# Optimization experiments

Hardware: AMD Instinct MI355X
Metric: run time of the kernel (lower is better)

The kernel has to match this reference:

```python
import jax, jax.numpy as jnp
import numpy as np

M, A, E, H = 2048, 64, 128, 256
NUM_BOND_TYPES, NUM_ATOM_TYPES = 4, 118

def setup_inputs() -> dict:
    key = jax.random.key(0)
    ks = jax.random.split(key, 12)
    s = 0.02
    return {
        'node_rep': jax.random.normal(ks[0], (M, A, H), jnp.float32),
        'edge_index': jax.random.randint(ks[1], (M, 2, E), 0, A, jnp.int32),
        'bond_type_target': jax.random.randint(ks[2], (M, E), 0, NUM_BOND_TYPES, jnp.int32),
        'atom_type_target': jax.random.randint(ks[3], (M, A), 0, NUM_ATOM_TYPES, jnp.int32),
        'Wp1': jax.random.normal(ks[4], (H, H), jnp.float32) * s, 'bp1': jnp.zeros((H,), jnp.float32),
        'Wp2': jax.random.normal(ks[5], (H, H), jnp.float32) * s, 'bp2': jnp.zeros((H,), jnp.float32),
        'Wb1': jax.random.normal(ks[6], (2 * H, H), jnp.float32) * s, 'bb1': jnp.zeros((H,), jnp.float32),
        'Wb2': jax.random.normal(ks[7], (H, NUM_BOND_TYPES), jnp.float32) * s, 'bb2': jnp.zeros((NUM_BOND_TYPES,), jnp.float32),
        'Wa1': jax.random.normal(ks[8], (H, H), jnp.float32) * s, 'ba1': jnp.zeros((H,), jnp.float32),
        'Wa2': jax.random.normal(ks[9], (H, NUM_ATOM_TYPES), jnp.float32) * s, 'ba2': jnp.zeros((NUM_ATOM_TYPES,), jnp.float32),
    }

def _mlp(x, W1, b1, W2, b2):
    return jnp.maximum(x @ W1 + b1, 0.0) @ W2 + b2

def reference(node_rep, edge_index, bond_type_target, atom_type_target,
              Wp1, bp1, Wp2, bp2, Wb1, bb1, Wb2, bb2, Wa1, ba1, Wa2, ba2):
    # bond_if_proj: per-atom 2-layer MLP (dropout=0 -> identity)  [M,A,H]
    proj = _mlp(node_rep, Wp1, bp1, Wp2, bp2)
    # gather bond endpoint reps: index_select over atoms per molecule  [M,E,H]
    start = jnp.take_along_axis(proj, edge_index[:, 0, :, None], axis=1)
    end = jnp.take_along_axis(proj, edge_index[:, 1, :, None], axis=1)
    bt_in = jnp.concatenate([start, end], axis=-1)            # [M,E,2H]
    bt_logits = _mlp(bt_in, Wb1, bb1, Wb2, bb2)               # [M,E,4]
    bt_logp = jax.nn.log_softmax(bt_logits, axis=-1)
    # per-molecule mean CE averaged over molecules == global mean (equal sizes)
    bond_type_loss = -jnp.mean(jnp.take_along_axis(bt_logp, bond_type_target[..., None], axis=-1))
    bond_type_acc = jnp.mean((jnp.argmax(bt_logits, axis=-1) == bond_type_target).astype(jnp.float32))
    # atom type classifier on raw node reps  [M,A,118]
    at_logits = _mlp(node_rep, Wa1, ba1, Wa2, ba2)
    at_logp = jax.nn.log_softmax(at_logits, axis=-1)
    atom_type_loss = -jnp.mean(jnp.take_along_axis(at_logp, atom_type_target[..., None], axis=-1))
    atom_type_acc = jnp.mean((jnp.argmax(at_logits, axis=-1) == atom_type_target).astype(jnp.float32))
    loss = 0.5 * bond_type_loss + 0.5 * atom_type_loss
    return loss, bond_type_acc, atom_type_acc
```

## Files before the change

### kernel.cpp

```cpp
#include <hip/hip_runtime.h>
#include <hip/hip_bf16.h>

typedef __bf16 bf16x8 __attribute__((ext_vector_type(8)));
typedef float f32x16 __attribute__((ext_vector_type(16)));

__device__ inline unsigned short f2bf(float f) {
  __hip_bfloat16 h = __float2bfloat16(f);
  return *reinterpret_cast<unsigned short*>(&h);
}
__device__ inline unsigned pack2bf(float a, float b) {
  return (unsigned)f2bf(a) | ((unsigned)f2bf(b) << 16);
}
__device__ inline uint2 pack4bf(float a, float b, float c, float d) {
  uint2 r; r.x = pack2bf(a, b); r.y = pack2bf(c, d); return r;
}
__device__ inline bf16x8 as_bf16x8(uint4 v) { return __builtin_bit_cast(bf16x8, v); }
__device__ inline float bitf(unsigned u) { return __builtin_bit_cast(float, u); }
__device__ inline f32x16 mfma16(bf16x8 a, bf16x8 b, f32x16 c) {
  return __builtin_amdgcn_mfma_f32_32x32x16_bf16(a, b, c, 0, 0, 0);
}

#define BROW(XB, KK)                                                           \
  ((XB) + ((((rw + l31) << 9) + ((KK) << 5) + (h << 4)) ^ swz))

#define GEMM8(XB, W1PTR, W2PTR)                                                \
  {                                                                            \
    const unsigned char* w1_ = (const unsigned char*)(W1PTR) +                 \
                               ((cw + l31) << 5) + (h << 4);                   \
    const unsigned char* w2_ = (const unsigned char*)(W2PTR) +                 \
                               ((cw + l31) << 5) + (h << 4);                   \
    u0 = zero; u1 = zero; v0 = zero; v1 = zero;                                \
    bf16x8 pB = *(const bf16x8*)BROW(XB, 0);                                   \
    uint4 pA0 = *(const uint4*)(w1_);                                          \
    uint4 pA1 = *(const uint4*)(w1_ + 1024);                                   \
    uint4 pC0 = *(const uint4*)(w2_);                                          \
    uint4 pC1 = *(const uint4*)(w2_ + 1024);                                   \
    _Pragma("clang loop unroll(disable)")                                      \
    for (int kk = 0; kk < 16; kk += 2) {                                       \
      bf16x8 qB = *(const bf16x8*)BROW(XB, kk + 1);                            \
      uint4 qA0 = *(const uint4*)(w1_ + ((kk + 1) << 13));                     \
      uint4 qA1 = *(const uint4*)(w1_ + ((kk + 1) << 13) + 1024);              \
      uint4 qC0 = *(const uint4*)(w2_ + ((kk + 1) << 13));                     \
      uint4 qC1 = *(const uint4*)(w2_ + ((kk + 1) << 13) + 1024);              \
      u0 = mfma16(as_bf16x8(pA0), pB, u0);                                     \
      u1 = mfma16(as_bf16x8(pA1), pB, u1);                                     \
      v0 = mfma16(as_bf16x8(pC0), pB, v0);                                     \
      v1 = mfma16(as_bf16x8(pC1), pB, v1);                                     \
      if (kk + 2 < 16) {                                                       \
        pB = *(const bf16x8*)BROW(XB, kk + 2);                                 \
        pA0 = *(const uint4*)(w1_ + ((kk + 2) << 13));                         \
        pA1 = *(const uint4*)(w1_ + ((kk + 2) << 13) + 1024);                  \
        pC0 = *(const uint4*)(w2_ + ((kk + 2) << 13));                         \
        pC1 = *(const uint4*)(w2_ + ((kk + 2) << 13) + 1024);                  \
      }                                                                        \
      u0 = mfma16(as_bf16x8(qA0), qB, u0);                                     \
      u1 = mfma16(as_bf16x8(qA1), qB, u1);                                     \
      v0 = mfma16(as_bf16x8(qC0), qB, v0);                                     \
      v1 = mfma16(as_bf16x8(qC1), qB, v1);                                     \
    }                                                                          \
  }

#define WB8(DB, ACC, C, BIASPTR)                                               \
  _Pragma("unroll")                                                            \
  for (int g = 0; g < 4; ++g) {                                                \
    int xr_ = rw + l31;                                                        \
    int col = cw + (C) * 32 + g * 8 + h * 4;                                   \
    float4 bb = *(const float4*)((BIASPTR) + col);                             \
    float v0_ = fmaxf(ACC[4 * g + 0] + bb.x, 0.f);                             \
    float v1_ = fmaxf(ACC[4 * g + 1] + bb.y, 0.f);                             \
    float v2_ = fmaxf(ACC[4 * g + 2] + bb.z, 0.f);                             \
    float v3_ = fmaxf(ACC[4 * g + 3] + bb.w, 0.f);                             \
    int off = ((xr_ << 9) + (col << 1)) ^ ((xr_ & 7) << 4);                    \
    *(uint2*)((DB) + off) = pack4bf(v0_, v1_, v2_, v3_);                       \
  }

#define WB8R(DB, ACC, C)                                                       \
  _Pragma("unroll")                                                            \
  for (int g = 0; g < 4; ++g) {                                                \
    int xr_ = rw + l31;                                                        \
    int col = cw + (C) * 32 + g * 8 + h * 4;                                   \
    int off = ((xr_ << 9) + (col << 1)) ^ ((xr_ & 7) << 4);                    \
    *(uint2*)((DB) + off) = pack4bf(ACC[4 * g + 0], ACC[4 * g + 1],            \
                                    ACC[4 * g + 2], ACC[4 * g + 3]);           \
  }

#define STAGE_X(DST, SRC)                                                      \
  _Pragma("unroll")                                                            \
  for (int it = 0; it < 4; ++it) {                                             \
    int lb = (it * 512 + tid) * 16;                                            \
    int d_ = lb ^ (((lb >> 9) & 7) << 4);                                      \
    const float4* s4 = (const float4*)((SRC) + (lb >> 1));                     \
    float4 f0 = s4[0], f1 = s4[1];                                             \
    uint4 v_ = { pack2bf(f0.x, f0.y), pack2bf(f0.z, f0.w),                     \
                 pack2bf(f1.x, f1.y), pack2bf(f1.z, f1.w) };                   \
    *(uint4*)((DST) + d_) = v_;                                                \
  }

__global__ __launch_bounds__(256) void k_pack(
    const float* __restrict__ wp1, const float* __restrict__ wa1,
    const float* __restrict__ wa2,
    unsigned short* __restrict__ dp1, unsigned short* __restrict__ da1,
    unsigned short* __restrict__ da2, float* __restrict__ accum)
{
  int b = blockIdx.x, tid = threadIdx.x;
  if (b == 0 && tid < 8) accum[tid] = 0.f;
  const float* src; unsigned short* dst; int e, logN, Nreal;
  if (b < 256)       { src = wp1; dst = dp1; e = b * 256 + tid;          logN = 8; Nreal = 256; }
  else if (b < 512)  { src = wa1; dst = da1; e = (b - 256) * 256 + tid;  logN = 8; Nreal = 256; }
  else               { src = wa2; dst = da2; e = (b - 512) * 256 + tid;  logN = 7; Nreal = 118; }
  int dk = e & 15;
  int rest = e >> 4;
  int n = rest & ((1 << logN) - 1);
  int kk = rest >> logN;
  int k = kk * 16 + dk;
  float v = (n < Nreal) ? src[k * Nreal + n] : 0.f;
  dst[e] = f2bf(v);
}

__global__ __launch_bounds__(256) void k_fold(
    const float* __restrict__ wp2, const float* __restrict__ wb1,
    const float* __restrict__ bp2, const float* __restrict__ bb1,
    unsigned short* __restrict__ dct, unsigned short* __restrict__ dcb,
    float* __restrict__ bias_e)
{
  int b = blockIdx.x, n = threadIdx.x;
  if (b < 512) {
    int k = b & 255;
    int off = (b < 256) ? 0 : 256;
    float s = 0.f;
    for (int t = 0; t < 256; ++t)
      s += wp2[k * 256 + t] * wb1[(t + off) * 256 + n];
    unsigned short* dst = (b < 256) ? dct : dcb;
    dst[((k >> 4) * 256 + n) * 16 + (k & 15)] = f2bf(s);
  } else {
    float s = bb1[n];
    for (int t = 0; t < 256; ++t)
      s += bp2[t] * (wb1[t * 256 + n] + wb1[(256 + t) * 256 + n]);
    bias_e[n] = s;
  }
}

__global__ __launch_bounds__(512, 4) void k_mol(
    const float* __restrict__ node, const int* __restrict__ eidx,
    const int* __restrict__ btt, const int* __restrict__ att,
    const unsigned short* __restrict__ wp1p, const float* __restrict__ bp1,
    const unsigned short* __restrict__ wctp, const unsigned short* __restrict__ wcbp,
    const float* __restrict__ bias_e, const float* __restrict__ wb2,
    const float* __restrict__ bb2,
    const unsigned short* __restrict__ wa1p, const float* __restrict__ ba1,
    const unsigned short* __restrict__ wa2p, const float* __restrict__ ba2,
    float* __restrict__ accum)
{
  __shared__ __align__(16) unsigned char bufA[32768];
  __shared__ __align__(16) unsigned char bufB[32768];
  __shared__ float s_bias[256];
  __shared__ float4 s_wb2[256];
  __shared__ float s_b2a[128];
  __shared__ float s_red[16];
  const int tid = threadIdx.x;
  const int lane = tid & 63;
  const int w = tid >> 6;
  const int l31 = lane & 31;
  const int h = lane >> 5;
  const int swz = (l31 & 7) << 4;
  const int rw = (w >> 2) * 32;
  const int cw = (w & 3) * 64;
  const int m = blockIdx.x;

  STAGE_X(bufA, node + (long)m * 16384);
  if (tid < 256) {
    s_bias[tid] = bias_e[tid];
    s_wb2[tid] = ((const float4*)wb2)[tid];
  }
  if (tid < 128) s_b2a[tid] = (tid < 118) ? ba2[tid] : 0.f;
  const int t_at = att[m * 64 + (tid >> 3)];
  __syncthreads();

  f32x16 zero = {};
  f32x16 u0, u1, v0, v1;

  GEMM8(bufA, wa1p, wp1p);
  WB8(bufB, u0, 0, ba1);
  WB8(bufB, u1, 1, ba1);
  __syncthreads();
  WB8(bufA, v0, 0, bp1);
  WB8(bufA, v1, 1, bp1);
  __syncthreads();

  f32x16 aL = zero;
  {
    const int cw2 = (w & 3) * 32;
    const unsigned char* wb_ = (const unsigned char*)wa2p +
                               ((cw2 + l31) << 5) + (h << 4);
    bf16x8 pB = *(const bf16x8*)BROW(bufB, 0);
    uint4 pA = *(const uint4*)(wb_);
    _Pragma("clang loop unroll(disable)")
    for (int kk = 0; kk < 16; kk += 2) {
      bf16x8 qB = *(const bf16x8*)BROW(bufB, kk + 1);
      uint4 qA = *(const uint4*)(wb_ + ((kk + 1) << 12));
      aL = mfma16(as_bf16x8(pA), pB, aL);
      if (kk + 2 < 16) {
        pB = *(const bf16x8*)BROW(bufB, kk + 2);
        pA = *(const uint4*)(wb_ + ((kk + 2) << 12));
      }
      aL = mfma16(as_bf16x8(qA), qB, aL);
    }
  }
  __syncthreads();

  {
    const int cw2 = (w & 3) * 32;
    const int r0 = rw + l31;
    #pragma unroll
    for (int q = 0; q < 16; ++q) {
      int col = cw2 + (q & 3) + 8 * (q >> 2) + 4 * h;
      if (col < 118)
        *(float*)(bufB + ((r0 << 9) + (((col << 2)) ^ ((r0 & 7) << 4)))) =
            aL[q] + s_b2a[col];
    }
  }
  __syncthreads();

  {
    const int row = tid >> 3, g8 = tid & 7;
    const unsigned char* lr = bufB + (row << 9);
    const int rswz = (row & 7) << 4;
    const int c0 = g8 * 15;
    const int cend = (g8 == 7) ? 118 : c0 + 15;
    float mx = -3.0e38f; int am = 127;
    for (int c = c0; c < cend; ++c) {
      float v = *(const float*)(lr + (((c << 2)) ^ rswz));
      if (v > mx) { mx = v; am = c; }
    }
    #pragma unroll
    for (int d = 1; d < 8; d <<= 1) {
      float mo = __shfl_xor(mx, d); int amo = __shfl_xor(am, d);
      if (mo > mx || (mo == mx && amo < am)) { mx = mo; am = amo; }
    }
    float s = 0.f, vt = 0.f;
    for (int c = c0; c < cend; ++c) {
      float v = *(const float*)(lr + (((c << 2)) ^ rswz));
      s += __expf(v - mx);
      if (c == t_at) vt = v;
    }
    #pragma unroll
    for (int d = 1; d < 8; d <<= 1) { s += __shfl_xor(s, d); vt += __shfl_xor(vt, d); }
    float ce = 0.f, cc = 0.f;
    if (g8 == 0) { ce = __logf(s) + mx - vt; cc = (am == t_at) ? 1.f : 0.f; }
    #pragma unroll
    for (int d = 8; d < 64; d <<= 1) { ce += __shfl_xor(ce, d); cc += __shfl_xor(cc, d); }
    #pragma unroll
    for (int d = 1; d < 8; d <<= 1) { ce += __shfl_xor(ce, d); cc += __shfl_xor(cc, d); }
    if (lane == 0) { s_red[w * 2] = ce; s_red[w * 2 + 1] = cc; }
  }

  GEMM8(bufA, wctp, wcbp);
  const int es = eidx[m * 256 + (tid >> 2)];
  const int ed = eidx[m * 256 + 128 + (tid >> 2)];
  const int etg = btt[m * 128 + (tid >> 2)];
  const float b20 = bb2[0], b21 = bb2[1], b22 = bb2[2], b23 = bb2[3];
  __syncthreads();
  if (tid == 0) {
    atomicAdd(accum + 2, s_red[0] + s_red[2] + s_red[4] + s_red[6] +
                         s_red[8] + s_red[10] + s_red[12] + s_red[14]);
    atomicAdd(accum + 3, s_red[1] + s_red[3] + s_red[5] + s_red[7] +
                         s_red[9] + s_red[11] + s_red[13] + s_red[15]);
  }
  WB8R(bufA, u0, 0);
  WB8R(bufA, u1, 1);
  WB8R(bufB, v0, 0);
  WB8R(bufB, v1, 1);
  __syncthreads();

  {
    const int qf = tid & 3;
    float lg0 = 0.f, lg1 = 0.f, lg2 = 0.f, lg3 = 0.f;
    #pragma unroll
    for (int j = 0; j < 8; ++j) {
      int c0 = qf * 64 + j * 8;
      int offS = ((es << 9) + (c0 << 1)) ^ ((es & 7) << 4);
      int offD = ((ed << 9) + (c0 << 1)) ^ ((ed & 7) << 4);
      uint4 us = *(const uint4*)(bufA + offS);
      uint4 ud = *(const uint4*)(bufB + offD);
      const unsigned* pu = (const unsigned*)&us;
      const unsigned* pv = (const unsigned*)&ud;
      #pragma unroll
      for (int q = 0; q < 4; ++q) {
        unsigned ua = pu[q], ub = pv[q];
        int c = c0 + 2 * q;
        float hlo = bitf(ua << 16) + bitf(ub << 16) + s_bias[c];
        float hhi = bitf(ua & 0xffff0000u) + bitf(ub & 0xffff0000u) + s_bias[c + 1];
        hlo = fmaxf(hlo, 0.f); hhi = fmaxf(hhi, 0.f);
        float4 w0 = s_wb2[c], w1 = s_wb2[c + 1];
        lg0 = fmaf(hlo, w0.x, fmaf(hhi, w1.x, lg0));
        lg1 = fmaf(hlo, w0.y, fmaf(hhi, w1.y, lg1));
        lg2 = fmaf(hlo, w0.z, fmaf(hhi, w1.z, lg2));
        lg3 = fmaf(hlo, w0.w, fmaf(hhi, w1.w, lg3));
      }
    }
    lg0 += __shfl_xor(lg0, 1); lg1 += __shfl_xor(lg1, 1);
    lg2 += __shfl_xor(lg2, 1); lg3 += __shfl_xor(lg3, 1);
    lg0 += __shfl_xor(lg0, 2); lg1 += __shfl_xor(lg1, 2);
    lg2 += __shfl_xor(lg2, 2); lg3 += __shfl_xor(lg3, 2);
    float ce = 0.f, cc = 0.f;
    if (qf == 0) {
      float l0 = lg0 + b20, l1 = lg1 + b21, l2 = lg2 + b22, l3 = lg3 + b23;
      int t = etg;
      int am = 0; float mx = l0;
      if (l1 > mx) { mx = l1; am = 1; }
      if (l2 > mx) { mx = l2; am = 2; }
      if (l3 > mx) { mx = l3; am = 3; }
      float s = __expf(l0 - mx) + __expf(l1 - mx) + __expf(l2 - mx) + __expf(l3 - mx);
      float lt = (t == 0) ? l0 : (t == 1) ? l1 : (t == 2) ? l2 : l3;
      ce = __logf(s) + mx - lt;
      cc = (am == t) ? 1.f : 0.f;
    }
    #pragma unroll
    for (int d = 1; d < 64; d <<= 1) { ce += __shfl_xor(ce, d); cc += __shfl_xor(cc, d); }
    if (lane == 0) { s_red[w * 2] = ce; s_red[w * 2 + 1] = cc; }
    __syncthreads();
    if (tid == 0) {
      atomicAdd(accum + 0, s_red[0] + s_red[2] + s_red[4] + s_red[6] +
                           s_red[8] + s_red[10] + s_red[12] + s_red[14]);
      atomicAdd(accum + 1, s_red[1] + s_red[3] + s_red[5] + s_red[7] +
                           s_red[9] + s_red[11] + s_red[13] + s_red[15]);
    }
  }
}

__global__ __launch_bounds__(64) void k_final(const float* __restrict__ accum,
                                              float* __restrict__ out)
{
  if (threadIdx.x == 0) {
    float bce = accum[0] / 262144.f;
    float bcc = accum[1] / 262144.f;
    float ace = accum[2] / 131072.f;
    float acc_ = accum[3] / 131072.f;
    out[0] = 0.5f * bce + 0.5f * ace;
    out[1] = bcc;
    out[2] = acc_;
  }
}

extern "C" void kernel_launch(void* const* d_in, const int* in_sizes, int n_in,
                              void* d_out, int out_size, void* d_ws, size_t ws_size,
                              hipStream_t stream)
{
  const float* node = (const float*)d_in[0];
  const int* eidx   = (const int*)d_in[1];
  const int* btt    = (const int*)d_in[2];
  const int* att    = (const int*)d_in[3];
  const float* Wp1 = (const float*)d_in[4];
  const float* bp1 = (const float*)d_in[5];
  const float* Wp2 = (const float*)d_in[6];
  const float* bp2 = (const float*)d_in[7];
  const float* Wb1 = (const float*)d_in[8];
  const float* bb1 = (const float*)d_in[9];
  const float* Wb2 = (const float*)d_in[10];
  const float* bb2 = (const float*)d_in[11];
  const float* Wa1 = (const float*)d_in[12];
  const float* ba1 = (const float*)d_in[13];
  const float* Wa2 = (const float*)d_in[14];
  const float* ba2 = (const float*)d_in[15];

  char* ws = (char*)d_ws;
  float* accum = (float*)ws;
  unsigned short* dp1 = (unsigned short*)(ws + 256);
  unsigned short* da1 = (unsigned short*)(ws + 131328);
  unsigned short* da2 = (unsigned short*)(ws + 262400);
  unsigned short* dct = (unsigned short*)(ws + 327936);
  unsigned short* dcb = (unsigned short*)(ws + 459008);
  float* bias_e       = (float*)(ws + 590080);

  k_pack<<<640, 256, 0, stream>>>(Wp1, Wa1, Wa2, dp1, da1, da2, accum);
  k_fold<<<513, 256, 0, stream>>>(Wp2, Wb1, bp2, bb1, dct, dcb, bias_e);
  k_mol<<<2048, 512, 0, stream>>>(node, eidx, btt, att, dp1, bp1, dct, dcb,
                                  bias_e, Wb2, bb2, da1, ba1, da2, ba2, accum);
  k_final<<<1, 64, 0, stream>>>(accum, (float*)d_out);
}
```

Before: 188.6 us.

## Process two molecules per block with 1024 threads and vectorize softmax LDS access

Each block now handles two molecules (128 atom rows) with 1024 threads, doubling the LDS buffers, so each weight tile loaded from global memory is reused across twice as many rows. The atom-logit writeback and the log-softmax scans switch from scalar to float4 LDS accesses. The block now uses about 136KB of LDS and 1024 threads, which may cut residency to one block per CU and limit latency hiding. The GEMM macros use 8 waves of row/column mapping (rw from w>>2), so whether the larger tile maps correctly to 16 waves is not visible here.

```diff
diff --git a/kernel.cpp b/kernel.cpp
--- a/kernel.cpp
+++ b/kernel.cpp
@@ -87,7 +87,7 @@
 #define STAGE_X(DST, SRC)                                                      \
   _Pragma("unroll")                                                            \
   for (int it = 0; it < 4; ++it) {                                             \
-    int lb = (it * 512 + tid) * 16;                                            \
+    int lb = (it * 1024 + tid) * 16;                                           \
     int d_ = lb ^ (((lb >> 9) & 7) << 4);                                      \
     const float4* s4 = (const float4*)((SRC) + (lb >> 1));                     \
     float4 f0 = s4[0], f1 = s4[1];                                             \
@@ -140,7 +140,7 @@
   }
 }
 
-__global__ __launch_bounds__(512, 4) void k_mol(
+__global__ __launch_bounds__(1024, 4) void k_mol(
     const float* __restrict__ node, const int* __restrict__ eidx,
     const int* __restrict__ btt, const int* __restrict__ att,
     const unsigned short* __restrict__ wp1p, const float* __restrict__ bp1,
@@ -151,12 +151,12 @@
     const unsigned short* __restrict__ wa2p, const float* __restrict__ ba2,
     float* __restrict__ accum)
 {
-  __shared__ __align__(16) unsigned char bufA[32768];
-  __shared__ __align__(16) unsigned char bufB[32768];
+  __shared__ __align__(16) unsigned char bufA[65536];
+  __shared__ __align__(16) unsigned char bufB[65536];
   __shared__ float s_bias[256];
   __shared__ float4 s_wb2[256];
   __shared__ float s_b2a[128];
-  __shared__ float s_red[16];
+  __shared__ float s_red[32];
   const int tid = threadIdx.x;
   const int lane = tid & 63;
   const int w = tid >> 6;
@@ -167,13 +167,13 @@
   const int cw = (w & 3) * 64;
   const int m = blockIdx.x;
 
-  STAGE_X(bufA, node + (long)m * 16384);
+  STAGE_X(bufA, node + (long)m * 32768);
   if (tid < 256) {
     s_bias[tid] = bias_e[tid];
     s_wb2[tid] = ((const float4*)wb2)[tid];
   }
   if (tid < 128) s_b2a[tid] = (tid < 118) ? ba2[tid] : 0.f;
-  const int t_at = att[m * 64 + (tid >> 3)];
+  const int t_at = att[m * 128 + (tid >> 3)];
   __syncthreads();
 
   f32x16 zero = {};
@@ -211,12 +211,16 @@
   {
     const int cw2 = (w & 3) * 32;
     const int r0 = rw + l31;
-    #pragma unroll
-    for (int q = 0; q < 16; ++q) {
-      int col = cw2 + (q & 3) + 8 * (q >> 2) + 4 * h;
-      if (col < 118)
-        *(float*)(bufB + ((r0 << 9) + (((col << 2)) ^ ((r0 & 7) << 4)))) =
-            aL[q] + s_b2a[col];
+    const int rx = (r0 & 7) << 4;
+    #pragma unroll
+    for (int g = 0; g < 4; ++g) {
+      int colb = cw2 + 8 * g + 4 * h;
+      uint4 val;
+      val.x = __builtin_bit_cast(unsigned, aL[4 * g + 0] + s_b2a[colb + 0]);
+      val.y = __builtin_bit_cast(unsigned, aL[4 * g + 1] + s_b2a[colb + 1]);
+      val.z = __builtin_bit_cast(unsigned, aL[4 * g + 2] + s_b2a[colb + 2]);
+      val.w = __builtin_bit_cast(unsigned, aL[4 * g + 3] + s_b2a[colb + 3]);
+      *(uint4*)(bufB + (((r0 << 9) + (colb << 2)) ^ rx)) = val;
     }
   }
   __syncthreads();
@@ -224,13 +228,19 @@
   {
     const int row = tid >> 3, g8 = tid & 7;
     const unsigned char* lr = bufB + (row << 9);
-    const int rswz = (row & 7) << 4;
-    const int c0 = g8 * 15;
-    const int cend = (g8 == 7) ? 118 : c0 + 15;
+    const int rx = (row & 7) << 4;
     float mx = -3.0e38f; int am = 127;
-    for (int c = c0; c < cend; ++c) {
-      float v = *(const float*)(lr + (((c << 2)) ^ rswz));
-      if (v > mx) { mx = v; am = c; }
+    #pragma unroll
+    for (int j = 0; j < 4; ++j) {
+      int ch = g8 + 8 * j;
+      if (ch < 30) {
+        float4 f = *(const float4*)(lr + (((ch << 4)) ^ rx));
+        int c = ch * 4;
+        if (f.x > mx) { mx = f.x; am = c; }
+        if (f.y > mx) { mx = f.y; am = c + 1; }
+        if (c + 2 < 118 && f.z > mx) { mx = f.z; am = c + 2; }
+        if (c + 3 < 118 && f.w > mx) { mx = f.w; am = c + 3; }
+      }
     }
     #pragma unroll
     for (int d = 1; d < 8; d <<= 1) {
@@ -238,33 +248,46 @@
       if (mo > mx || (mo == mx && amo < am)) { mx = mo; am = amo; }
     }
     float s = 0.f, vt = 0.f;
-    for (int c = c0; c < cend; ++c) {
-      float v = *(const float*)(lr + (((c << 2)) ^ rswz));
-      s += __expf(v - mx);
-      if (c == t_at) vt = v;
+    #pragma unroll
+    for (int j = 0; j < 4; ++j) {
+      int ch = g8 + 8 * j;
+      if (ch < 30) {
+        float4 f = *(const float4*)(lr + (((ch << 4)) ^ rx));
+        int c = ch * 4;
+        s += __expf(f.x - mx);
+        s += __expf(f.y - mx);
+        if (c + 2 < 118) s += __expf(f.z - mx);
+        if (c + 3 < 118) s += __expf(f.w - mx);
+        if (c == t_at) vt = f.x;
+        if (c + 1 == t_at) vt = f.y;
+        if (c + 2 == t_at) vt = f.z;
+        if (c + 3 == t_at) vt = f.w;
+      }
     }
     #pragma unroll
     for (int d = 1; d < 8; d <<= 1) { s += __shfl_xor(s, d); vt += __shfl_xor(vt, d); }
     float ce = 0.f, cc = 0.f;
     if (g8 == 0) { ce = __logf(s) + mx - vt; cc = (am == t_at) ? 1.f : 0.f; }
     #pragma unroll
-    for (int d = 8; d < 64; d <<= 1) { ce += __shfl_xor(ce, d); cc += __shfl_xor(cc, d); }
-    #pragma unroll
-    for (int d = 1; d < 8; d <<= 1) { ce += __shfl_xor(ce, d); cc += __shfl_xor(cc, d); }
+    for (int d = 1; d < 64; d <<= 1) { ce += __shfl_xor(ce, d); cc += __shfl_xor(cc, d); }
     if (lane == 0) { s_red[w * 2] = ce; s_red[w * 2 + 1] = cc; }
   }
 
   GEMM8(bufA, wctp, wcbp);
-  const int es = eidx[m * 256 + (tid >> 2)];
-  const int ed = eidx[m * 256 + 128 + (tid >> 2)];
-  const int etg = btt[m * 128 + (tid >> 2)];
+  const int e_ = tid >> 2;
+  const int gmol = e_ >> 7;
+  const int ee = e_ & 127;
+  const int es = gmol * 64 + eidx[(2 * m + gmol) * 256 + ee];
+  const int ed = gmol * 64 + eidx[(2 * m + gmol) * 256 + 128 + ee];
+  const int etg = btt[(2 * m + gmol) * 128 + ee];
   const float b20 = bb2[0], b21 = bb2[1], b22 = bb2[2], b23 = bb2[3];
   __syncthreads();
   if (tid == 0) {
-    atomicAdd(accum + 2, s_red[0] + s_red[2] + s_red[4] + s_red[6] +
-                         s_red[8] + s_red[10] + s_red[12] + s_red[14]);
-    atomicAdd(accum + 3, s_red[1] + s_red[3] + s_red[5] + s_red[7] +
-                         s_red[9] + s_red[11] + s_red[13] + s_red[15]);
+    float sa = 0.f, sb = 0.f;
+    #pragma unroll
+    for (int i = 0; i < 16; ++i) { sa += s_red[2 * i]; sb += s_red[2 * i + 1]; }
+    atomicAdd(accum + 2, sa);
+    atomicAdd(accum + 3, sb);
   }
   WB8R(bufA, u0, 0);
   WB8R(bufA, u1, 1);
@@ -320,10 +343,11 @@
     if (lane == 0) { s_red[w * 2] = ce; s_red[w * 2 + 1] = cc; }
     __syncthreads();
     if (tid == 0) {
-      atomicAdd(accum + 0, s_red[0] + s_red[2] + s_red[4] + s_red[6] +
-                           s_red[8] + s_red[10] + s_red[12] + s_red[14]);
-      atomicAdd(accum + 1, s_red[1] + s_red[3] + s_red[5] + s_red[7] +
-                           s_red[9] + s_red[11] + s_red[13] + s_red[15]);
+      float sa = 0.f, sb = 0.f;
+      #pragma unroll
+      for (int i = 0; i < 16; ++i) { sa += s_red[2 * i]; sb += s_red[2 * i + 1]; }
+      atomicAdd(accum + 0, sa);
+      atomicAdd(accum + 1, sb);
     }
   }
 }
@@ -374,7 +398,7 @@
 
   k_pack<<<640, 256, 0, stream>>>(Wp1, Wa1, Wa2, dp1, da1, da2, accum);
   k_fold<<<513, 256, 0, stream>>>(Wp2, Wb1, bp2, bb1, dct, dcb, bias_e);
-  k_mol<<<2048, 512, 0, stream>>>(node, eidx, btt, att, dp1, bp1, dct, dcb,
-                                  bias_e, Wb2, bb2, da1, ba1, da2, ba2, accum);
+  k_mol<<<1024, 1024, 0, stream>>>(node, eidx, btt, att, dp1, bp1, dct, dcb,
+                                   bias_e, Wb2, bb2, da1, ba1, da2, ba2, accum);
   k_final<<<1, 64, 0, stream>>>(accum, (float*)d_out);
 }
```

New measurement: 197.1 us. 4.5% more time.
